# Performance work log

Measured on AMD Instinct MI355X. Metric: run time of the kernel, lower is better.

Reference implementation:

```python
import jax, jax.numpy as jnp
import numpy as np

DIM = 2048
N_HEADS = 16
N_KV_HEADS = 4
HEAD_DIM = DIM // N_HEADS  # 128
B, N = 2, 2048
SCALE = HEAD_DIM ** -0.5


def apply_rotary_emb(x, cos, sin):
    # x: [b, n, h, d]; cos/sin: [1, n, 1, d//2]
    d = x.shape[-1] // 2
    x1, x2 = x[..., :d], x[..., d:]
    y1 = x1 * cos + x2 * sin
    y2 = x2 * cos - x1 * sin
    return jnp.concatenate((y1, y2), axis=-1).astype(x.dtype)


def setup_inputs() -> dict:
    key = jax.random.key(0)
    ks = jax.random.split(key, 8)
    x = jax.random.normal(ks[0], (B, N, DIM), dtype=jnp.float32)
    cos = jax.random.uniform(ks[1], (1, N, 1, HEAD_DIM // 2), dtype=jnp.float32)
    sin = jax.random.uniform(ks[2], (1, N, 1, HEAD_DIM // 2), dtype=jnp.float32)
    attn_mask = jnp.ones((B, N, N), dtype=bool)
    s = 1.0 / np.sqrt(DIM)
    wq = jax.random.normal(ks[3], (N_HEADS * HEAD_DIM, DIM), dtype=jnp.float32) * s
    wkv = jax.random.normal(ks[4], (2 * N_KV_HEADS * HEAD_DIM, DIM), dtype=jnp.float32) * s
    wo_w = jax.random.normal(ks[5], (DIM, N_HEADS * HEAD_DIM), dtype=jnp.float32) * s
    wo_b = jax.random.normal(ks[6], (DIM,), dtype=jnp.float32) * 0.01
    return {"x": x, "cos": cos, "sin": sin, "attn_mask": attn_mask,
            "wq": wq, "wkv": wkv, "wo_w": wo_w, "wo_b": wo_b}


def reference(x, cos, sin, attn_mask, wq, wkv, wo_w, wo_b):
    b, n, _ = x.shape
    q = jnp.einsum('bnd,ed->bne', x, wq)              # [b, n, H*hd]
    kv = jnp.einsum('bnd,ed->bne', x, wkv)            # [b, n, 2*Hkv*hd]
    k, v = jnp.split(kv, 2, axis=-1)
    q = q.reshape(b, n, N_HEADS, HEAD_DIM)
    k = k.reshape(b, n, N_KV_HEADS, HEAD_DIM)
    v = v.reshape(b, n, N_KV_HEADS, HEAD_DIM)
    q = apply_rotary_emb(q, cos, sin)
    k = apply_rotary_emb(k, cos, sin)
    q = q.transpose(0, 2, 1, 3)   # [b, H, n, hd]
    k = k.transpose(0, 2, 1, 3)   # [b, Hkv, n, hd]
    v = v.transpose(0, 2, 1, 3)
    r = N_HEADS // N_KV_HEADS
    # einops repeat 'b h n d -> b (r h) n d': tile the whole head block r times
    k = jnp.tile(k, (1, r, 1, 1))
    v = jnp.tile(v, (1, r, 1, 1))
    attn = jnp.einsum('bhqd,bhkd->bhqk', q, k) * SCALE
    neg = jnp.logical_not(attn_mask)[:, None, :, :].astype(attn.dtype) * -1e9
    attn = jax.nn.softmax(attn + neg, axis=-1)
    out = jnp.einsum('bhqk,bhkd->bhqd', attn, v)
    out = out.transpose(0, 2, 1, 3).reshape(b, n, N_HEADS * HEAD_DIM)
    return jnp.einsum('bne,de->bnd', out, wo_w) + wo_b
```

## Files before the change

kernel.cpp:

```cpp
#include <hip/hip_runtime.h>
#include <hip/hip_bf16.h>

#define DIMM   2048
#define NHEADS 16
#define NKVH   4
#define HD     128
#define BATCH  2
#define SEQ    2048
#define KEXP2  (0.08838834764831845f * 1.44269504088896340736f)

using bf16 = __hip_bfloat16;
typedef __attribute__((ext_vector_type(8))) short frag8;
typedef __attribute__((ext_vector_type(4))) short short4v;
typedef __attribute__((ext_vector_type(4))) float floatx4;
typedef __attribute__((ext_vector_type(16))) float floatx16;
typedef unsigned int u32;

static __device__ __forceinline__ float bf2f(bf16 x) { return __bfloat162float(x); }
static __device__ __forceinline__ bf16  f2bf(float x) { return __float2bfloat16(x); }

static __device__ __forceinline__ void stage16(const void* g, void* l) {
    __builtin_amdgcn_global_load_lds(
        (const __attribute__((address_space(1))) u32*)g,
        (__attribute__((address_space(3))) u32*)l,
        16, 0, 0);
}

__global__ void cast_all(const float* __restrict__ x, const float* __restrict__ wq,
                         const float* __restrict__ wkv, const float* __restrict__ wo,
                         bf16* __restrict__ xb, bf16* __restrict__ wqb,
                         bf16* __restrict__ wkvb, bf16* __restrict__ wob)
{
    int blk = blockIdx.x;
    const float* src; bf16* dst; int base;
    if (blk < 4096)      { src = x;   dst = xb;   base = blk; }
    else if (blk < 6144) { src = wq;  dst = wqb;  base = blk - 4096; }
    else if (blk < 7168) { src = wkv; dst = wkvb; base = blk - 6144; }
    else                 { src = wo;  dst = wob;  base = blk - 7168; }
    int i = (base * 256 + threadIdx.x) * 8;
    float4 a = *(const float4*)(src + i);
    float4 b = *(const float4*)(src + i + 4);
    __align__(16) bf16 t[8];
    t[0] = f2bf(a.x); t[1] = f2bf(a.y); t[2] = f2bf(a.z); t[3] = f2bf(a.w);
    t[4] = f2bf(b.x); t[5] = f2bf(b.y); t[6] = f2bf(b.z); t[7] = f2bf(b.w);
    *(frag8*)(dst + i) = *(const frag8*)t;
}

__global__ __launch_bounds__(256)
void gemm_qkv(const bf16* __restrict__ A, const bf16* __restrict__ wqb,
              const bf16* __restrict__ wkvb, bf16* __restrict__ qout,
              bf16* __restrict__ kvout,
              const float* __restrict__ cosb, const float* __restrict__ sinb)
{
    __shared__ __align__(16) bf16 As[128 * 32];
    __shared__ __align__(16) bf16 Bs[128 * 32];

    const int tm     = blockIdx.x & 31;
    const int tn_all = blockIdx.x >> 5;
    const bf16* B; bf16* C; int Nn, tn; bool isq;
    if (tn_all < 16) { B = wqb;  C = qout;  Nn = DIMM; tn = tn_all;      isq = true;  }
    else             { B = wkvb; C = kvout; Nn = 1024; tn = tn_all - 16; isq = false; }

    const int tid  = threadIdx.x;
    const int lane = tid & 63;
    const int wave = tid >> 6;
    const int l16  = lane & 15;
    const int quad = lane >> 4;

    floatx4 acc[2][8];
#pragma unroll
    for (int i = 0; i < 2; i++)
#pragma unroll
        for (int j = 0; j < 8; j++) acc[i][j] = (floatx4)(0.0f);

    const int srow_in = tid >> 2;
    const int sswz    = (tid >> 3) & 3;
    const int sblog   = (tid & 3) ^ sswz;

    const bf16* Abase = A + (size_t)(tm * 128) * DIMM + sblog * 8;
    const bf16* Bbase = B + (size_t)(tn * 128) * DIMM + sblog * 8;

    for (int k0 = 0; k0 < DIMM; k0 += 32) {
        __syncthreads();
#pragma unroll
        for (int c = 0; c < 2; c++) {
            int r = c * 64 + srow_in;
            stage16(Abase + (size_t)r * DIMM + k0, &As[c * 2048 + tid * 8]);
            stage16(Bbase + (size_t)r * DIMM + k0, &Bs[c * 2048 + tid * 8]);
        }
        __syncthreads();

        frag8 af[2], bfr[8];
#pragma unroll
        for (int i = 0; i < 2; i++) {
            int r = wave * 32 + i * 16 + l16;
            int p = quad ^ ((r >> 1) & 3);
            af[i] = *(const frag8*)(&As[r * 32 + p * 8]);
        }
#pragma unroll
        for (int j = 0; j < 8; j++) {
            int r = j * 16 + l16;
            int p = quad ^ ((r >> 1) & 3);
            bfr[j] = *(const frag8*)(&Bs[r * 32 + p * 8]);
        }
#pragma unroll
        for (int i = 0; i < 2; i++)
#pragma unroll
            for (int j = 0; j < 8; j++)
                acc[i][j] = __builtin_amdgcn_mfma_f32_16x16x32_bf16(af[i], bfr[j], acc[i][j], 0, 0, 0);
    }

    const int crow0 = tm * 128 + wave * 32;
    const int ccol0 = tn * 128;
    bool do_rope = isq || (tn < NKVH);
    if (do_rope) {
#pragma unroll
        for (int i = 0; i < 2; i++) {
#pragma unroll
            for (int r = 0; r < 4; r++) {
                int row = crow0 + i * 16 + quad * 4 + r;
                int n = row & (SEQ - 1);
#pragma unroll
                for (int j = 0; j < 4; j++) {
                    int dd = j * 16 + l16;
                    float c = cosb[n * 64 + dd];
                    float s = sinb[n * 64 + dd];
                    float a1 = acc[i][j][r], a2 = acc[i][j + 4][r];
                    float y1 = a1 * c + a2 * s;
                    float y2 = a2 * c - a1 * s;
                    if (isq) { y1 *= KEXP2; y2 *= KEXP2; }
                    C[(size_t)row * Nn + ccol0 + dd]      = f2bf(y1);
                    C[(size_t)row * Nn + ccol0 + dd + 64] = f2bf(y2);
                }
            }
        }
    } else {
#pragma unroll
        for (int i = 0; i < 2; i++)
#pragma unroll
            for (int j = 0; j < 8; j++) {
                int col = ccol0 + j * 16 + l16;
                int rbase = crow0 + i * 16 + quad * 4;
#pragma unroll
                for (int r = 0; r < 4; r++)
                    C[(size_t)(rbase + r) * Nn + col] = f2bf(acc[i][j][r]);
            }
    }
}

__global__ __launch_bounds__(256)
void gemm_out(const bf16* __restrict__ A, const bf16* __restrict__ B,
              float* __restrict__ C, const float* __restrict__ bias)
{
    __shared__ __align__(16) bf16 As[128 * 32];
    __shared__ __align__(16) bf16 Bs[128 * 32];

    const int tm = blockIdx.x & 31;
    const int tn = blockIdx.x >> 5;

    const int tid  = threadIdx.x;
    const int lane = tid & 63;
    const int wave = tid >> 6;
    const int wm   = wave >> 1;
    const int wn   = wave & 1;
    const int l16  = lane & 15;
    const int quad = lane >> 4;

    floatx4 acc[4][4];
#pragma unroll
    for (int i = 0; i < 4; i++)
#pragma unroll
        for (int j = 0; j < 4; j++) acc[i][j] = (floatx4)(0.0f);

    const int srow_in = tid >> 2;
    const int sswz    = (tid >> 3) & 3;
    const int sblog   = (tid & 3) ^ sswz;

    const bf16* Abase = A + (size_t)(tm * 128) * DIMM + sblog * 8;
    const bf16* Bbase = B + (size_t)(tn * 128) * DIMM + sblog * 8;

    for (int k0 = 0; k0 < DIMM; k0 += 32) {
        __syncthreads();
#pragma unroll
        for (int c = 0; c < 2; c++) {
            int r = c * 64 + srow_in;
            stage16(Abase + (size_t)r * DIMM + k0, &As[c * 2048 + tid * 8]);
            stage16(Bbase + (size_t)r * DIMM + k0, &Bs[c * 2048 + tid * 8]);
        }
        __syncthreads();

        frag8 af[4], bfr[4];
#pragma unroll
        for (int i = 0; i < 4; i++) {
            int r = wm * 64 + i * 16 + l16;
            int p = quad ^ ((r >> 1) & 3);
            af[i] = *(const frag8*)(&As[r * 32 + p * 8]);
        }
#pragma unroll
        for (int j = 0; j < 4; j++) {
            int r = wn * 64 + j * 16 + l16;
            int p = quad ^ ((r >> 1) & 3);
            bfr[j] = *(const frag8*)(&Bs[r * 32 + p * 8]);
        }
#pragma unroll
        for (int i = 0; i < 4; i++)
#pragma unroll
            for (int j = 0; j < 4; j++)
                acc[i][j] = __builtin_amdgcn_mfma_f32_16x16x32_bf16(af[i], bfr[j], acc[i][j], 0, 0, 0);
    }

    const int crow0 = tm * 128 + wm * 64;
    const int ccol0 = tn * 128 + wn * 64;
#pragma unroll
    for (int i = 0; i < 4; i++) {
#pragma unroll
        for (int j = 0; j < 4; j++) {
            int col = ccol0 + j * 16 + l16;
            float bv = bias[col];
            int rbase = crow0 + i * 16 + quad * 4;
#pragma unroll
            for (int r = 0; r < 4; r++)
                C[(size_t)(rbase + r) * DIMM + col] = acc[i][j][r] + bv;
        }
    }
}

__global__ void vtrans(const bf16* __restrict__ kvb, bf16* __restrict__ vtb)
{
    __shared__ __align__(16) bf16 T[128 * 72];
    const int blk = blockIdx.x;
    const int b   = blk >> 7;
    const int kh  = (blk >> 5) & 3;
    const int kt  = blk & 31;
    const int tid = threadIdx.x;

    const bf16* vbase = kvb + (size_t)b * SEQ * 1024 + 512 + kh * HD;
    const int vkey  = (tid & 15) * 4;
    const int vdgrp = tid >> 4;
    frag8 vv[4];
#pragma unroll
    for (int j = 0; j < 4; j++)
        vv[j] = *(const frag8*)(vbase + (size_t)(kt * 64 + vkey + j) * 1024 + vdgrp * 8);
#pragma unroll
    for (int dd = 0; dd < 8; dd++) {
        int d = vdgrp * 8 + dd;
        short4v sv = { vv[0][dd], vv[1][dd], vv[2][dd], vv[3][dd] };
        *(short4v*)(&T[d * 72 + vkey]) = sv;
    }
    __syncthreads();
    bf16* obase = vtb + (size_t)((b * 4 + kh) * 128) * 2048 + kt * 64;
#pragma unroll
    for (int c = 0; c < 4; c++) {
        int idx = c * 256 + tid;
        int d = idx >> 3, kb = idx & 7;
        *(frag8*)(obase + (size_t)d * 2048 + kb * 8) = *(const frag8*)(&T[d * 72 + kb * 8]);
    }
}

__global__ __launch_bounds__(512, 2)
void flash_attn(const bf16* __restrict__ qb, const bf16* __restrict__ kvb,
                const bf16* __restrict__ vtb, bf16* __restrict__ ob)
{
    __shared__ __align__(16) bf16 Ks[2][64 * 128];
    __shared__ __align__(16) bf16 Vt[2][128 * 64];

    const int qt = blockIdx.x;
    const int bh = blockIdx.y;
    const int b  = bh / NHEADS;
    const int h  = bh % NHEADS;
    const int kh = h % NKVH;

    const int tid  = threadIdx.x;
    const int lane = tid & 63;
    const int wave = tid >> 6;
    const int l32  = lane & 31;
    const int hi   = lane >> 5;

    const int qrow0 = qt * 256 + wave * 32;
    frag8 qf[8];
    {
        const bf16* qp = qb + (size_t)(b * SEQ + qrow0 + l32) * DIMM + h * HD + hi * 8;
#pragma unroll
        for (int ks = 0; ks < 8; ks++)
            qf[ks] = *(const frag8*)(qp + ks * 16);
    }

    floatx16 o0 = (floatx16)(0.0f), o1 = (floatx16)(0.0f);
    floatx16 o2 = (floatx16)(0.0f), o3 = (floatx16)(0.0f);
    float lsum = 0.0f;

    const bf16* kbase  = kvb + (size_t)b * SEQ * 1024 + kh * HD;
    const bf16* vtbase = vtb + (size_t)((b * 4 + kh) * 128) * 2048;

    const int ksr = tid >> 4;
    const int ksb = (tid & 15) ^ (ksr & 15);
    const int vr  = tid >> 3;

#pragma unroll
    for (int c = 0; c < 2; c++)
        stage16(kbase + (size_t)(c * 32 + ksr) * 1024 + ksb * 8,
                &Ks[0][c * 4096 + tid * 8]);
#pragma unroll
    for (int c = 0; c < 2; c++) {
        int d = c * 64 + vr;
        int blk = (tid & 7) ^ (d & 7);
        stage16(vtbase + (size_t)d * 2048 + blk * 8,
                &Vt[0][c * 4096 + tid * 8]);
    }
    asm volatile("s_waitcnt vmcnt(0)" ::: "memory");
    __builtin_amdgcn_s_barrier();

    int x = 0;
    for (int kt = 0; kt < SEQ / 64; ++kt) {
        if (kt + 1 < SEQ / 64) {
#pragma unroll
            for (int c = 0; c < 2; c++)
                stage16(kbase + (size_t)((kt + 1) * 64 + c * 32 + ksr) * 1024 + ksb * 8,
                        &Ks[x ^ 1][c * 4096 + tid * 8]);
#pragma unroll
            for (int c = 0; c < 2; c++) {
                int d = c * 64 + vr;
                int blk = (tid & 7) ^ (d & 7);
                stage16(vtbase + (size_t)d * 2048 + (kt + 1) * 64 + blk * 8,
                        &Vt[x ^ 1][c * 4096 + tid * 8]);
            }
        }

        floatx16 sc0 = (floatx16)(0.0f), sc1 = (floatx16)(0.0f);
        __builtin_amdgcn_s_setprio(1);
#pragma unroll
        for (int ks = 0; ks < 8; ks++) {
            int pos = (2 * ks + hi) ^ (l32 & 15);
            frag8 kf0 = *(const frag8*)(&Ks[x][l32 * 128 + pos * 8]);
            frag8 kf1 = *(const frag8*)(&Ks[x][(32 + l32) * 128 + pos * 8]);
            sc0 = __builtin_amdgcn_mfma_f32_32x32x16_bf16(kf0, qf[ks], sc0, 0, 0, 0);
            sc1 = __builtin_amdgcn_mfma_f32_32x32x16_bf16(kf1, qf[ks], sc1, 0, 0, 0);
        }
        __builtin_amdgcn_s_setprio(0);

        float pe0[16], pe1[16];
#pragma unroll
        for (int r = 0; r < 16; r++) { pe0[r] = exp2f(sc0[r]); lsum += pe0[r]; }
#pragma unroll
        for (int r = 0; r < 16; r++) { pe1[r] = exp2f(sc1[r]); lsum += pe1[r]; }

#define PV_STEP(nn, pe)                                                          \
        {                                                                        \
            u32 w0, w1, w2, w3;                                                  \
            asm("v_cvt_pk_bf16_f32 %0, %1, %2" : "=v"(w0)                        \
                : "v"(pe[((nn)&1)*8 + 0]), "v"(pe[((nn)&1)*8 + 1]));             \
            asm("v_cvt_pk_bf16_f32 %0, %1, %2" : "=v"(w1)                        \
                : "v"(pe[((nn)&1)*8 + 2]), "v"(pe[((nn)&1)*8 + 3]));             \
            asm("v_cvt_pk_bf16_f32 %0, %1, %2" : "=v"(w2)                        \
                : "v"(pe[((nn)&1)*8 + 4]), "v"(pe[((nn)&1)*8 + 5]));             \
            asm("v_cvt_pk_bf16_f32 %0, %1, %2" : "=v"(w3)                        \
                : "v"(pe[((nn)&1)*8 + 6]), "v"(pe[((nn)&1)*8 + 7]));             \
            asm("v_permlane32_swap_b32 %0, %1" : "+v"(w0), "+v"(w2));            \
            asm("v_permlane32_swap_b32 %0, %1" : "+v"(w1), "+v"(w3));            \
            union { u32 d[4]; frag8 f; } pa;                                     \
            pa.d[0] = w0; pa.d[1] = w1; pa.d[2] = w2; pa.d[3] = w3;              \
            int vpos = (2 * (nn) + hi) ^ (l32 & 7);                              \
            frag8 vf0 = *(const frag8*)(&Vt[x][(l32)       * 64 + vpos * 8]);    \
            frag8 vf1 = *(const frag8*)(&Vt[x][(32 + l32)  * 64 + vpos * 8]);    \
            frag8 vf2 = *(const frag8*)(&Vt[x][(64 + l32)  * 64 + vpos * 8]);    \
            frag8 vf3 = *(const frag8*)(&Vt[x][(96 + l32)  * 64 + vpos * 8]);    \
            __builtin_amdgcn_s_setprio(1);                                       \
            o0 = __builtin_amdgcn_mfma_f32_32x32x16_bf16(pa.f, vf0, o0, 0, 0, 0);\
            o1 = __builtin_amdgcn_mfma_f32_32x32x16_bf16(pa.f, vf1, o1, 0, 0, 0);\
            o2 = __builtin_amdgcn_mfma_f32_32x32x16_bf16(pa.f, vf2, o2, 0, 0, 0);\
            o3 = __builtin_amdgcn_mfma_f32_32x32x16_bf16(pa.f, vf3, o3, 0, 0, 0);\
            __builtin_amdgcn_s_setprio(0);                                       \
        }
        PV_STEP(0, pe0)
        PV_STEP(1, pe0)
        PV_STEP(2, pe1)
        PV_STEP(3, pe1)
#undef PV_STEP

        asm volatile("s_waitcnt vmcnt(0)" ::: "memory");
        __builtin_amdgcn_s_barrier();
        x ^= 1;
    }

    float lt = lsum + __shfl_xor(lsum, 32);
    float invq[16];
#pragma unroll
    for (int r = 0; r < 16; r++) {
        int rowq = (r & 3) + 8 * (r >> 2) + 4 * hi;
        invq[r] = 1.0f / __shfl(lt, rowq);
    }

#pragma unroll
    for (int r = 0; r < 16; r++) {
        int row = qrow0 + (r & 3) + 8 * (r >> 2) + 4 * hi;
        bf16* op = ob + (size_t)(b * SEQ + row) * DIMM + h * HD + l32;
        op[0]  = f2bf(o0[r] * invq[r]);
        op[32] = f2bf(o1[r] * invq[r]);
        op[64] = f2bf(o2[r] * invq[r]);
        op[96] = f2bf(o3[r] * invq[r]);
    }
}

extern "C" void kernel_launch(void* const* d_in, const int* in_sizes, int n_in,
                              void* d_out, int out_size, void* d_ws, size_t ws_size,
                              hipStream_t stream)
{
    const float* x    = (const float*)d_in[0];
    const float* cosb = (const float*)d_in[1];
    const float* sinb = (const float*)d_in[2];
    const float* wq   = (const float*)d_in[4];
    const float* wkv  = (const float*)d_in[5];
    const float* wo_w = (const float*)d_in[6];
    const float* wo_b = (const float*)d_in[7];
    float* out = (float*)d_out;

    const int M = BATCH * SEQ;
    const int NX   = M * DIMM;
    const int NWQ  = DIMM * DIMM;
    const int NWKV = 1024 * DIMM;
    const int NWO  = DIMM * DIMM;

    bf16* xb    = (bf16*)d_ws;
    bf16* wqb   = xb    + NX;
    bf16* wkvb  = wqb   + NWQ;
    bf16* wob   = wkvb  + NWKV;
    bf16* qbuf  = wob   + NWO;
    bf16* kvbuf = qbuf  + (size_t)M * DIMM;
    bf16* vtbuf = kvbuf + (size_t)M * 1024;
    bf16* abuf  = vtbuf + (size_t)BATCH * NKVH * HD * SEQ;

    cast_all<<<9216, 256, 0, stream>>>(x, wq, wkv, wo_w, xb, wqb, wkvb, wob);
    gemm_qkv<<<24 * 32, 256, 0, stream>>>(xb, wqb, wkvb, qbuf, kvbuf, cosb, sinb);
    vtrans<<<256, 256, 0, stream>>>(kvbuf, vtbuf);
    flash_attn<<<dim3(SEQ / 256, BATCH * NHEADS), 512, 0, stream>>>(qbuf, kvbuf, vtbuf, abuf);
    gemm_out<<<16 * 32, 256, 0, stream>>>(abuf, wob, out, wo_b);
}
```

Measured before the change: 331.6 us.

## Shrink attention blocks to 2 waves and load V fragments directly from global

```diff
diff --git a/kernel.cpp b/kernel.cpp
--- a/kernel.cpp
+++ b/kernel.cpp
@@ -257,12 +257,11 @@
     }
 }
 
-__global__ __launch_bounds__(512, 2)
+__global__ __launch_bounds__(128, 2)
 void flash_attn(const bf16* __restrict__ qb, const bf16* __restrict__ kvb,
                 const bf16* __restrict__ vtb, bf16* __restrict__ ob)
 {
     __shared__ __align__(16) bf16 Ks[2][64 * 128];
-    __shared__ __align__(16) bf16 Vt[2][128 * 64];
 
     const int qt = blockIdx.x;
     const int bh = blockIdx.y;
@@ -276,7 +275,7 @@
     const int l32  = lane & 31;
     const int hi   = lane >> 5;
 
-    const int qrow0 = qt * 256 + wave * 32;
+    const int qrow0 = qt * 64 + wave * 32;
     frag8 qf[8];
     {
         const bf16* qp = qb + (size_t)(b * SEQ + qrow0 + l32) * DIMM + h * HD + hi * 8;
@@ -292,39 +291,28 @@
     const bf16* kbase  = kvb + (size_t)b * SEQ * 1024 + kh * HD;
     const bf16* vtbase = vtb + (size_t)((b * 4 + kh) * 128) * 2048;
 
-    const int ksr = tid >> 4;
-    const int ksb = (tid & 15) ^ (ksr & 15);
-    const int vr  = tid >> 3;
-
-#pragma unroll
-    for (int c = 0; c < 2; c++)
-        stage16(kbase + (size_t)(c * 32 + ksr) * 1024 + ksb * 8,
-                &Ks[0][c * 4096 + tid * 8]);
-#pragma unroll
-    for (int c = 0; c < 2; c++) {
-        int d = c * 64 + vr;
-        int blk = (tid & 7) ^ (d & 7);
-        stage16(vtbase + (size_t)d * 2048 + blk * 8,
-                &Vt[0][c * 4096 + tid * 8]);
-    }
+    const int ksr   = tid >> 4;
+    const int ksb_e = (tid & 15) ^ ksr;
+    const int ksb_o = (tid & 15) ^ (8 + ksr);
+
+#define STAGEK(kt_, buf_)                                                      \
+    {                                                                          \
+        _Pragma("unroll")                                                      \
+        for (int c = 0; c < 8; c++) {                                          \
+            int row = c * 8 + ksr;                                             \
+            int kb  = (c & 1) ? ksb_o : ksb_e;                                 \
+            stage16(kbase + (size_t)((kt_) * 64 + row) * 1024 + kb * 8,        \
+                    &Ks[buf_][c * 1024 + tid * 8]);                            \
+        }                                                                      \
+    }
+
+    STAGEK(0, 0)
     asm volatile("s_waitcnt vmcnt(0)" ::: "memory");
     __builtin_amdgcn_s_barrier();
 
     int x = 0;
     for (int kt = 0; kt < SEQ / 64; ++kt) {
-        if (kt + 1 < SEQ / 64) {
-#pragma unroll
-            for (int c = 0; c < 2; c++)
-                stage16(kbase + (size_t)((kt + 1) * 64 + c * 32 + ksr) * 1024 + ksb * 8,
-                        &Ks[x ^ 1][c * 4096 + tid * 8]);
-#pragma unroll
-            for (int c = 0; c < 2; c++) {
-                int d = c * 64 + vr;
-                int blk = (tid & 7) ^ (d & 7);
-                stage16(vtbase + (size_t)d * 2048 + (kt + 1) * 64 + blk * 8,
-                        &Vt[x ^ 1][c * 4096 + tid * 8]);
-            }
-        }
+        if (kt + 1 < SEQ / 64) STAGEK(kt + 1, x ^ 1)
 
         floatx16 sc0 = (floatx16)(0.0f), sc1 = (floatx16)(0.0f);
         __builtin_amdgcn_s_setprio(1);
@@ -338,13 +326,31 @@
         }
         __builtin_amdgcn_s_setprio(0);
 
+        const bf16* vp = vtbase + (size_t)l32 * 2048 + kt * 64 + hi * 8;
+        frag8 v0_0 = *(const frag8*)(vp);
+        frag8 v0_1 = *(const frag8*)(vp + 32 * 2048);
+        frag8 v0_2 = *(const frag8*)(vp + 64 * 2048);
+        frag8 v0_3 = *(const frag8*)(vp + 96 * 2048);
+        frag8 v1_0 = *(const frag8*)(vp + 16);
+        frag8 v1_1 = *(const frag8*)(vp + 32 * 2048 + 16);
+        frag8 v1_2 = *(const frag8*)(vp + 64 * 2048 + 16);
+        frag8 v1_3 = *(const frag8*)(vp + 96 * 2048 + 16);
+        frag8 v2_0 = *(const frag8*)(vp + 32);
+        frag8 v2_1 = *(const frag8*)(vp + 32 * 2048 + 32);
+        frag8 v2_2 = *(const frag8*)(vp + 64 * 2048 + 32);
+        frag8 v2_3 = *(const frag8*)(vp + 96 * 2048 + 32);
+        frag8 v3_0 = *(const frag8*)(vp + 48);
+        frag8 v3_1 = *(const frag8*)(vp + 32 * 2048 + 48);
+        frag8 v3_2 = *(const frag8*)(vp + 64 * 2048 + 48);
+        frag8 v3_3 = *(const frag8*)(vp + 96 * 2048 + 48);
+
         float pe0[16], pe1[16];
 #pragma unroll
         for (int r = 0; r < 16; r++) { pe0[r] = exp2f(sc0[r]); lsum += pe0[r]; }
 #pragma unroll
         for (int r = 0; r < 16; r++) { pe1[r] = exp2f(sc1[r]); lsum += pe1[r]; }
 
-#define PV_STEP(nn, pe)                                                          \
+#define PV_STEP(nn, pe, va, vb, vc, vd)                                          \
         {                                                                        \
             u32 w0, w1, w2, w3;                                                  \
             asm("v_cvt_pk_bf16_f32 %0, %1, %2" : "=v"(w0)                        \
@@ -359,28 +365,24 @@
             asm("v_permlane32_swap_b32 %0, %1" : "+v"(w1), "+v"(w3));            \
             union { u32 d[4]; frag8 f; } pa;                                     \
             pa.d[0] = w0; pa.d[1] = w1; pa.d[2] = w2; pa.d[3] = w3;              \
-            int vpos = (2 * (nn) + hi) ^ (l32 & 7);                              \
-            frag8 vf0 = *(const frag8*)(&Vt[x][(l32)       * 64 + vpos * 8]);    \
-            frag8 vf1 = *(const frag8*)(&Vt[x][(32 + l32)  * 64 + vpos * 8]);    \
-            frag8 vf2 = *(const frag8*)(&Vt[x][(64 + l32)  * 64 + vpos * 8]);    \
-            frag8 vf3 = *(const frag8*)(&Vt[x][(96 + l32)  * 64 + vpos * 8]);    \
             __builtin_amdgcn_s_setprio(1);                                       \
-            o0 = __builtin_amdgcn_mfma_f32_32x32x16_bf16(pa.f, vf0, o0, 0, 0, 0);\
-            o1 = __builtin_amdgcn_mfma_f32_32x32x16_bf16(pa.f, vf1, o1, 0, 0, 0);\
-            o2 = __builtin_amdgcn_mfma_f32_32x32x16_bf16(pa.f, vf2, o2, 0, 0, 0);\
-            o3 = __builtin_amdgcn_mfma_f32_32x32x16_bf16(pa.f, vf3, o3, 0, 0, 0);\
+            o0 = __builtin_amdgcn_mfma_f32_32x32x16_bf16(pa.f, va, o0, 0, 0, 0); \
+            o1 = __builtin_amdgcn_mfma_f32_32x32x16_bf16(pa.f, vb, o1, 0, 0, 0); \
+            o2 = __builtin_amdgcn_mfma_f32_32x32x16_bf16(pa.f, vc, o2, 0, 0, 0); \
+            o3 = __builtin_amdgcn_mfma_f32_32x32x16_bf16(pa.f, vd, o3, 0, 0, 0); \
             __builtin_amdgcn_s_setprio(0);                                       \
         }
-        PV_STEP(0, pe0)
-        PV_STEP(1, pe0)
-        PV_STEP(2, pe1)
-        PV_STEP(3, pe1)
+        PV_STEP(0, pe0, v0_0, v0_1, v0_2, v0_3)
+        PV_STEP(1, pe0, v1_0, v1_1, v1_2, v1_3)
+        PV_STEP(2, pe1, v2_0, v2_1, v2_2, v2_3)
+        PV_STEP(3, pe1, v3_0, v3_1, v3_2, v3_3)
 #undef PV_STEP
 
         asm volatile("s_waitcnt vmcnt(0)" ::: "memory");
         __builtin_amdgcn_s_barrier();
         x ^= 1;
     }
+#undef STAGEK
 
     float lt = lsum + __shfl_xor(lsum, 32);
     float invq[16];
@@ -432,6 +434,6 @@
     cast_all<<<9216, 256, 0, stream>>>(x, wq, wkv, wo_w, xb, wqb, wkvb, wob);
     gemm_qkv<<<24 * 32, 256, 0, stream>>>(xb, wqb, wkvb, qbuf, kvbuf, cosb, sinb);
     vtrans<<<256, 256, 0, stream>>>(kvbuf, vtbuf);
-    flash_attn<<<dim3(SEQ / 256, BATCH * NHEADS), 512, 0, stream>>>(qbuf, kvbuf, vtbuf, abuf);
+    flash_attn<<<dim3(SEQ / 64, BATCH * NHEADS), 128, 0, stream>>>(qbuf, kvbuf, vtbuf, abuf);
     gemm_out<<<16 * 32, 256, 0, stream>>>(abuf, wob, out, wo_b);
 }
```

Measured after the change: 386.1 us. 1.16x slower.
